# Performance work log

Measured on AMD Instinct MI355X. Metric: run time of the kernel, lower is better.

## Reference

```python
import jax, jax.numpy as jnp
import numpy as np

HEADS = 8
KD = 64  # key_dim
VD = 64  # value_dim


def _conv1x1(W, b, x):
    # 1x1 conv == per-pixel matmul over channels. W: [out, in], x: [b, in, h, w]
    return jnp.einsum('oc,bchw->bohw', W, x) + b[:, None, None]


def setup_inputs() -> dict:
    key = jax.random.key(0)
    ks = jax.random.split(key, 9)
    B, C, H, W = 4, 128, 128, 128
    s = 0.02
    return {
        'x':  jax.random.normal(ks[0], (B, C, H, W), jnp.float32),
        'Wq': jax.random.normal(ks[1], (KD * HEADS, C), jnp.float32) * s,
        'bq': jax.random.normal(ks[2], (KD * HEADS,), jnp.float32) * s,
        'Wk': jax.random.normal(ks[3], (KD * HEADS, C), jnp.float32) * s,
        'bk': jax.random.normal(ks[4], (KD * HEADS,), jnp.float32) * s,
        'Wv': jax.random.normal(ks[5], (VD * HEADS, C), jnp.float32) * s,
        'bv': jax.random.normal(ks[6], (VD * HEADS,), jnp.float32) * s,
        'Wo': jax.random.normal(ks[7], (C, VD * HEADS), jnp.float32) * s,
        'bo': jax.random.normal(ks[8], (C,), jnp.float32) * s,
    }


def reference(x, Wq, bq, Wk, bk, Wv, bv, Wo, bo):
    B, C, H, W = x.shape
    n = H * W
    scale = KD ** -0.25
    # projections -> [b, heads, dim, n]
    q = _conv1x1(Wq, bq, x).reshape(B, HEADS, KD, n) * scale
    k = _conv1x1(Wk, bk, x).reshape(B, HEADS, KD, n) * scale
    v = _conv1x1(Wv, bv, x).reshape(B, HEADS, VD, n)
    # linear attention: softmax k over tokens (n), softmax q over key dim (d)
    k = jax.nn.softmax(k, axis=-1)
    q = jax.nn.softmax(q, axis=-2)
    ctx = jnp.einsum('bhdn,bhen->bhde', k, v)   # [b, h, kd, vd] small context
    out = jnp.einsum('bhdn,bhde->bhen', q, ctx)  # [b, h, vd, n]
    out = out.reshape(B, HEADS * VD, H, W)
    return _conv1x1(Wo, bo, out)
```

## Files before the change

### kernel.cpp

```cpp
#include <hip/hip_runtime.h>

typedef unsigned short u16;
typedef __bf16 bf16x8 __attribute__((ext_vector_type(8)));
typedef float f32x4 __attribute__((ext_vector_type(4)));

#define N_ 16384
#define SCALE 0.35355339059327379f

__device__ __forceinline__ u16 f2bf(float f){
  union { float f; unsigned int i; } v; v.f = f;
  unsigned int b = v.i;
  return (u16)((b + 0x7FFFu + ((b >> 16) & 1u)) >> 16);
}
__device__ __forceinline__ unsigned int cvtpk(float a, float b){
  unsigned int r;
  asm("v_cvt_pk_bf16_f32 %0, %1, %2" : "=v"(r) : "v"(a), "v"(b));
  return r;
}

__global__ __launch_bounds__(256) void pconvx(const float* __restrict__ x,
    u16* __restrict__ xt, const float* __restrict__ Wq,
    const float* __restrict__ bq, const float* __restrict__ Wk,
    const float* __restrict__ bk, const float* __restrict__ Wv,
    const float* __restrict__ bv, u16* __restrict__ wkvf, u16* __restrict__ wqf,
    float* __restrict__ bkv, float* __restrict__ bqs){
  const int tid = threadIdx.x;
  const int bid = blockIdx.x;
  if (bid < 512){
    const int b = bid >> 7;
    const int kq = tid >> 6;
    const int t0 = (bid & 127) * 128 + 2 * (tid & 63);
    const float* xp = x + (size_t)(b * 128 + kq * 32) * N_ + t0;
    u16* dst = xt + (size_t)(b * N_ + t0) * 128;
#pragma unroll
    for (int gi = 0; gi < 4; gi++){
      float2 v[8];
#pragma unroll
      for (int j = 0; j < 8; j++)
        v[j] = *(const float2*)(xp + (size_t)(gi * 8 + j) * N_);
      const int g = kq * 4 + gi;
      {
        uint4 o;
        o.x = cvtpk(v[0].x, v[1].x); o.y = cvtpk(v[2].x, v[3].x);
        o.z = cvtpk(v[4].x, v[5].x); o.w = cvtpk(v[6].x, v[7].x);
        *(uint4*)(dst + ((g ^ (t0 & 15)) * 8)) = o;
      }
      {
        uint4 o;
        o.x = cvtpk(v[0].y, v[1].y); o.y = cvtpk(v[2].y, v[3].y);
        o.z = cvtpk(v[4].y, v[5].y); o.w = cvtpk(v[6].y, v[7].y);
        const int t = t0 + 1;
        *(uint4*)(dst + 128 + ((g ^ (t & 15)) * 8)) = o;
      }
    }
    return;
  }
  const int T = (bid - 512) * 256 + tid;
  if (T < 1024){
    int jj = T & 127, h = T >> 7;
    bkv[T] = (jj < 64) ? SCALE * bk[h * 64 + jj] : bv[h * 64 + jj - 64];
  } else if (T < 1536){
    bqs[T - 1024] = SCALE * bq[T - 1024];
  }
  const float* src; float sc; u16* dst;
  if (T < 16384){
    int l = T & 63, f = T >> 6;
    int ks = f & 3, jt = (f >> 2) & 7, h = f >> 5;
    int jj = 16 * jt + (l & 15);
    int k0 = ks * 32 + (l >> 4) * 8;
    if (jj < 64){ src = Wk + (size_t)(h * 64 + jj) * 128 + k0; sc = SCALE; }
    else        { src = Wv + (size_t)(h * 64 + jj - 64) * 128 + k0; sc = 1.f; }
    dst = wkvf + (size_t)f * 512 + l * 8;
  } else {
    int T2 = T - 16384;
    int l = T2 & 63, f = T2 >> 6;
    int ks = f & 3, dt = (f >> 2) & 3, h = f >> 4;
    int d = 16 * dt + (l & 15);
    int k0 = ks * 32 + (l >> 4) * 8;
    src = Wq + (size_t)(h * 64 + d) * 128 + k0; sc = SCALE;
    dst = wqf + (size_t)f * 512 + l * 8;
  }
  float4 a = *(const float4*)src, c = *(const float4*)(src + 4);
  ushort4 o0, o1;
  o0.x = f2bf(sc * a.x); o0.y = f2bf(sc * a.y); o0.z = f2bf(sc * a.z); o0.w = f2bf(sc * a.w);
  o1.x = f2bf(sc * c.x); o1.y = f2bf(sc * c.y); o1.z = f2bf(sc * c.z); o1.w = f2bf(sc * c.w);
  *(ushort4*)dst = o0; *(ushort4*)(dst + 4) = o1;
}

__global__ __launch_bounds__(256, 2) void kvctx(const u16* __restrict__ xt,
    const u16* __restrict__ wkvf, const float* __restrict__ bkv,
    float* __restrict__ pctx, float* __restrict__ prs){
  __shared__ u16 smem[32768];
  const int tid = threadIdx.x;
  const int chunk = blockIdx.x, h = blockIdx.y, b = blockIdx.z;
  const int w = tid >> 6, l = tid & 63, r15 = l & 15, q = l >> 4;
  const int th = w & 1, jh = w >> 1;

  bf16x8 wf[4][4];
#pragma unroll
  for (int ni = 0; ni < 4; ni++)
#pragma unroll
    for (int ks = 0; ks < 4; ks++)
      wf[ni][ks] = *(const bf16x8*)(wkvf +
          (size_t)((h * 8 + 4 * jh + ni) * 4 + ks) * 512 + l * 8);
  float barr[4];
#pragma unroll
  for (int ni = 0; ni < 4; ni++)
    barr[ni] = bkv[h * 128 + jh * 64 + 16 * ni + r15];

  const size_t tok0 = (size_t)b * N_ + chunk * 512;
  const char* gbase = (const char*)(xt + tok0 * 128);
  u16* sekv = smem + 16384;

#define STAGE(sub_)                                                            \
  {                                                                            \
    const char* gs = gbase + (size_t)(sub_)*32768 + w * 8192 + l * 16;         \
    char* ls = (char*)smem + w * 8192;                                         \
    _Pragma("unroll")                                                          \
    for (int p = 0; p < 8; p++)                                                \
      __builtin_amdgcn_global_load_lds(                                        \
          (const __attribute__((address_space(1))) void*)(gs + p * 1024),      \
          (__attribute__((address_space(3))) void*)(ls + p * 1024), 16, 0, 0); \
  }

  STAGE(0);
  __syncthreads();

  f32x4 acc2[4][4] = {};
  float rs[4] = {0.f, 0.f, 0.f, 0.f};

  for (int sub = 0; sub < 4; sub++){
    f32x4 acc1[4][4] = {};
#pragma unroll
    for (int ks = 0; ks < 4; ks++){
      bf16x8 xa[4];
#pragma unroll
      for (int mi = 0; mi < 4; mi++){
        int t = th * 64 + 16 * mi + r15;
        xa[mi] = *(const bf16x8*)&smem[t * 128 + (((ks * 4 + q) ^ r15) * 8)];
      }
#pragma unroll
      for (int mi = 0; mi < 4; mi++)
#pragma unroll
        for (int ni = 0; ni < 4; ni++)
          acc1[mi][ni] = __builtin_amdgcn_mfma_f32_16x16x32_bf16(
              xa[mi], wf[ni][ks], acc1[mi][ni], 0, 0, 0);
    }
    asm volatile("s_waitcnt lgkmcnt(0)" ::: "memory");
    __builtin_amdgcn_s_barrier();
    if (sub < 3) STAGE(sub + 1);
#pragma unroll
    for (int ni = 0; ni < 4; ni++){
      const float bb = barr[ni];
      const int j = jh * 64 + 16 * ni + r15;
      float ps = 0.f;
#pragma unroll
      for (int mi = 0; mi < 4; mi++){
        float vals[4];
#pragma unroll
        for (int r = 0; r < 4; r++) vals[r] = acc1[mi][ni][r] + bb;
        if (jh == 0){
#pragma unroll
          for (int r = 0; r < 4; r++){ vals[r] = __expf(vals[r]); ps += vals[r]; }
        }
        uint2 pk;
        pk.x = cvtpk(vals[0], vals[1]);
        pk.y = cvtpk(vals[2], vals[3]);
        int g8 = 16 * th + 4 * mi + q;
        int g8s = g8 ^ (2 * r15);
        *(uint2*)&sekv[j * 128 + g8s * 4] = pk;
      }
      if (jh == 0){
        ps += __shfl_xor(ps, 16); ps += __shfl_xor(ps, 32);
        rs[ni] += ps;
      }
    }
    asm volatile("s_waitcnt lgkmcnt(0)" ::: "memory");
    __builtin_amdgcn_s_barrier();
    {
      bf16x8 ka[4], va[4];
      const int g8s = (8 * w + 2 * q) ^ (2 * r15);
#pragma unroll
      for (int mi2 = 0; mi2 < 4; mi2++){
        int d = 16 * mi2 + r15;
        ka[mi2] = *(const bf16x8*)&sekv[d * 128 + g8s * 4];
      }
#pragma unroll
      for (int ni2 = 0; ni2 < 4; ni2++){
        int e = 16 * ni2 + r15;
        va[ni2] = *(const bf16x8*)&sekv[(64 + e) * 128 + g8s * 4];
      }
#pragma unroll
      for (int mi2 = 0; mi2 < 4; mi2++)
#pragma unroll
        for (int ni2 = 0; ni2 < 4; ni2++)
          acc2[mi2][ni2] = __builtin_amdgcn_mfma_f32_16x16x32_bf16(
              ka[mi2], va[ni2], acc2[mi2][ni2], 0, 0, 0);
    }
    __syncthreads();
  }
#undef STAGE
  float* fb = (float*)smem;
#pragma unroll
  for (int mi2 = 0; mi2 < 4; mi2++)
#pragma unroll
    for (int ni2 = 0; ni2 < 4; ni2++)
#pragma unroll
      for (int r = 0; r < 4; r++){
        int d = 16 * mi2 + 4 * q + r, e = 16 * ni2 + r15;
        fb[w * 4096 + d * 64 + e] = acc2[mi2][ni2][r];
      }
  __syncthreads();
  {
    float* dst = pctx + ((size_t)((b * 8 + h) * 32 + chunk)) * 4096 + tid * 16;
#pragma unroll
    for (int i = 0; i < 4; i++){
      int o = tid * 16 + 4 * i;
      float4 a = *(const float4*)(fb + o);
      float4 c = *(const float4*)(fb + 4096 + o);
      float4 d = *(const float4*)(fb + 8192 + o);
      float4 e = *(const float4*)(fb + 12288 + o);
      float4 s;
      s.x = a.x + c.x + d.x + e.x; s.y = a.y + c.y + d.y + e.y;
      s.z = a.z + c.z + d.z + e.z; s.w = a.w + c.w + d.w + e.w;
      *(float4*)(dst + 4 * i) = s;
    }
  }
  if (jh == 0 && q == 0){
    float* rb = prs + ((size_t)((b * 8 + h) * 32 + chunk)) * 128 + th * 64;
#pragma unroll
    for (int ni = 0; ni < 4; ni++) rb[16 * ni + r15] = rs[ni];
  }
}

__global__ __launch_bounds__(256) void redmker(const float* __restrict__ pctx,
    const float* __restrict__ prs, const float* __restrict__ Wo,
    u16* __restrict__ mtf){
  __shared__ float ctxh8[8][68];
  __shared__ float woht[64][132];
  __shared__ float rsh[8];
  const int tid = threadIdx.x;
  const int bh = blockIdx.x, s = blockIdx.y;
  const int h = bh & 7;
  {
    const int e4 = tid & 15, r0 = tid >> 4;
#pragma unroll
    for (int p = 0; p < 8; p++){
      int c = r0 + p * 16;
      float4 v = *(const float4*)(Wo + (size_t)c * 512 + h * 64 + 4 * e4);
      woht[4 * e4 + 0][c] = v.x; woht[4 * e4 + 1][c] = v.y;
      woht[4 * e4 + 2][c] = v.z; woht[4 * e4 + 3][c] = v.w;
    }
  }
  {
    const float* base = pctx + (size_t)bh * 131072 + s * 512 + tid * 2;
    float2 a = {0.f, 0.f};
#pragma unroll 4
    for (int c = 0; c < 32; c++){
      float2 v = *(const float2*)(base + c * 4096);
      a.x += v.x; a.y += v.y;
    }
    const int i = tid * 2;
    ctxh8[i >> 6][i & 63] = a.x;
    ctxh8[(i + 1) >> 6][(i + 1) & 63] = a.y;
  }
  {
    const int dl = tid >> 5, c = tid & 31;
    const int dg = s * 8 + dl;
    const float* rb = prs + (size_t)bh * 4096 + c * 128;
    float v = rb[dg] + rb[64 + dg];
    v += __shfl_xor(v, 1);  v += __shfl_xor(v, 2);
    v += __shfl_xor(v, 4);  v += __shfl_xor(v, 8);
    v += __shfl_xor(v, 16);
    if (c == 0) rsh[dl] = v;
  }
  __syncthreads();
  const int dl = tid >> 5, c0 = (tid & 31) * 4;
  const int d = s * 8 + dl;
  const float inv = 1.f / rsh[dl];
  float acc[4] = {0.f, 0.f, 0.f, 0.f};
  for (int e = 0; e < 64; e++){
    float cv = ctxh8[dl][e];
#pragma unroll
    for (int j = 0; j < 4; j++) acc[j] += cv * woht[e][c0 + j];
  }
  const int ks = d >> 5, lq = ((d >> 3) & 3) << 4, el = d & 7;
#pragma unroll
  for (int j = 0; j < 4; j++){
    int c = c0 + j;
    mtf[((size_t)(bh * 8 + (c >> 4)) * 2 + ks) * 512 + ((c & 15) | lq) * 8 + el]
        = f2bf(inv * acc[j]);
  }
}

__global__ __launch_bounds__(256, 3) void qout(const u16* __restrict__ xt,
    const u16* __restrict__ wqf, const float* __restrict__ bqs,
    const u16* __restrict__ mtf, const float* __restrict__ bo,
    float* __restrict__ out){
  __shared__ u16 smWq[8192];
  __shared__ u16 smWm[8192];
  __shared__ u16 smP[4][16 * 64];
  const int tid = threadIdx.x;
  const int tt = blockIdx.x, b = blockIdx.y;
  const int w = tid >> 6, l = tid & 63, r15 = l & 15, q = l >> 4;
  const int t0 = tt * 64;
  const int m7 = 2 * (r15 & 7);
  const int t = t0 + w * 16 + r15;

  bf16x8 xb[4];
#pragma unroll
  for (int ks = 0; ks < 4; ks++)
    xb[ks] = *(const bf16x8*)(xt + (size_t)(b * N_ + t) * 128 +
                              (((ks * 4 + q) ^ r15) * 8));

  u16* sp = smP[w];
  f32x4 acc3[8] = {};
  for (int h = 0; h < 8; h++){
    {
      const char* gsrc = (w < 2)
          ? (const char*)(wqf + (size_t)h * 8192) + w * 8192 + l * 16
          : (const char*)(mtf + (size_t)(b * 8 + h) * 8192) + (w - 2) * 8192 + l * 16;
      char* ldst = (w < 2) ? (char*)smWq + w * 8192
                           : (char*)smWm + (w - 2) * 8192;
#pragma unroll
      for (int p = 0; p < 8; p++)
        __builtin_amdgcn_global_load_lds(
            (const __attribute__((address_space(1))) void*)(gsrc + p * 1024),
            (__attribute__((address_space(3))) void*)(ldst + p * 1024), 16, 0, 0);
    }
    __syncthreads();

    float bq_[4][4];
#pragma unroll
    for (int mi = 0; mi < 4; mi++){
      float4 v = *(const float4*)(bqs + h * 64 + 16 * mi + 4 * q);
      bq_[mi][0] = v.x; bq_[mi][1] = v.y; bq_[mi][2] = v.z; bq_[mi][3] = v.w;
    }
    f32x4 acc1[4] = {};
#pragma unroll
    for (int ks = 0; ks < 4; ks++){
      bf16x8 wqv[4];
#pragma unroll
      for (int mi = 0; mi < 4; mi++)
        wqv[mi] = *(const bf16x8*)&smWq[(mi * 4 + ks) * 512 + l * 8];
#pragma unroll
      for (int mi = 0; mi < 4; mi++)
        acc1[mi] = __builtin_amdgcn_mfma_f32_16x16x32_bf16(
            wqv[mi], xb[ks], acc1[mi], 0, 0, 0);
    }
    {
      float ps = 0.f;
#pragma unroll
      for (int mi = 0; mi < 4; mi++)
#pragma unroll
        for (int r = 0; r < 4; r++){
          float e = __expf(acc1[mi][r] + bq_[mi][r]);
          acc1[mi][r] = e; ps += e;
        }
      ps += __shfl_xor(ps, 16); ps += __shfl_xor(ps, 32);
      const float ci = 1.f / ps;
#pragma unroll
      for (int mi = 0; mi < 4; mi++){
        uint2 pk;
        pk.x = cvtpk(acc1[mi][0] * ci, acc1[mi][1] * ci);
        pk.y = cvtpk(acc1[mi][2] * ci, acc1[mi][3] * ci);
        int g8s = (4 * mi + q) ^ m7;
        *(uint2*)&sp[r15 * 64 + g8s * 4] = pk;
      }
    }
#pragma unroll
    for (int ks2 = 0; ks2 < 2; ks2++){
      const int g8s = (8 * ks2 + 2 * q) ^ m7;
      bf16x8 pb = *(const bf16x8*)&sp[r15 * 64 + g8s * 4];
#pragma unroll
      for (int mm = 0; mm < 8; mm++){
        bf16x8 mf = *(const bf16x8*)&smWm[(mm * 2 + ks2) * 512 + l * 8];
        acc3[mm] = __builtin_amdgcn_mfma_f32_16x16x32_bf16(
            mf, pb, acc3[mm], 0, 0, 0);
      }
    }
    if (h < 7) __syncthreads();
  }
#pragma unroll
  for (int mi = 0; mi < 8; mi++){
    float4 bv = *(const float4*)(bo + 16 * mi + 4 * q);
    float bs[4] = {bv.x, bv.y, bv.z, bv.w};
#pragma unroll
    for (int r = 0; r < 4; r++){
      int c = 16 * mi + 4 * q + r;
      out[(size_t)(b * 128 + c) * N_ + t] = acc3[mi][r] + bs[r];
    }
  }
}

extern "C" void kernel_launch(void* const* d_in, const int* in_sizes, int n_in,
                              void* d_out, int out_size, void* d_ws, size_t ws_size,
                              hipStream_t stream){
  const float* x  = (const float*)d_in[0];
  const float* Wq = (const float*)d_in[1];
  const float* bq = (const float*)d_in[2];
  const float* Wk = (const float*)d_in[3];
  const float* bk = (const float*)d_in[4];
  const float* Wv = (const float*)d_in[5];
  const float* bv = (const float*)d_in[6];
  const float* Wo = (const float*)d_in[7];
  const float* bo = (const float*)d_in[8];
  float* out = (float*)d_out;

  char* ws = (char*)d_ws;
  u16*   xt     = (u16*)ws;
  u16*   wkvf   = (u16*)(ws + 16777216);
  u16*   wqf    = (u16*)(ws + 17039360);
  u16*   mtf    = (u16*)(ws + 17170432);
  float* bkv    = (float*)(ws + 17694720);
  float* bqs    = (float*)(ws + 17698816);
  float* pctx   = (float*)(ws + 18233344);
  float* prs    = (float*)(ws + 35010560);

  pconvx <<<608, 256, 0, stream>>>(x, xt, Wq, bq, Wk, bk, Wv, bv,
                                   wkvf, wqf, bkv, bqs);
  kvctx  <<<dim3(32, 8, 4), 256, 0, stream>>>(xt, wkvf, bkv, pctx, prs);
  redmker<<<dim3(32, 8), 256, 0, stream>>>(pctx, prs, Wo, mtf);
  qout   <<<dim3(256, 4), 256, 0, stream>>>(xt, wqf, bqs, mtf, bo, out);
}
```

Measured before the change: 170.5 us.

## Halve kvctx grid with larger token chunks and balance softmax exp across waves

Each kvctx block now processes 1024 tokens (8 sub-stages) instead of 512, so the grid shrinks from 32 to 16 chunks per (b,h). This halves the partial-context writes and the reduction reads in redmker. Output-column tiles are also reassigned so every wave handles two K tiles (which need exp) and two V tiles. Previously only half the waves did all the exp work. The cost is fewer blocks (512 total), which may under-fill the GPU, and a longer serial loop per block.

New measurement: 163.6 us, median of 2. 1.04x faster.

```diff
diff --git a/kernel.cpp b/kernel.cpp
--- a/kernel.cpp
+++ b/kernel.cpp
@@ -92,23 +92,27 @@
     float* __restrict__ pctx, float* __restrict__ prs){
   __shared__ u16 smem[32768];
   const int tid = threadIdx.x;
-  const int chunk = blockIdx.x, h = blockIdx.y, b = blockIdx.z;
+  const int cp = blockIdx.x, h = blockIdx.y, b = blockIdx.z;
   const int w = tid >> 6, l = tid & 63, r15 = l & 15, q = l >> 4;
   const int th = w & 1, jh = w >> 1;
 
+  int jt_[4];
+#pragma unroll
+  for (int ni = 0; ni < 4; ni++) jt_[ni] = (ni < 2) ? (2 * jh + ni) : (2 + 2 * jh + ni);
+
   bf16x8 wf[4][4];
 #pragma unroll
   for (int ni = 0; ni < 4; ni++)
 #pragma unroll
     for (int ks = 0; ks < 4; ks++)
       wf[ni][ks] = *(const bf16x8*)(wkvf +
-          (size_t)((h * 8 + 4 * jh + ni) * 4 + ks) * 512 + l * 8);
+          (size_t)((h * 8 + jt_[ni]) * 4 + ks) * 512 + l * 8);
   float barr[4];
 #pragma unroll
   for (int ni = 0; ni < 4; ni++)
-    barr[ni] = bkv[h * 128 + jh * 64 + 16 * ni + r15];
-
-  const size_t tok0 = (size_t)b * N_ + chunk * 512;
+    barr[ni] = bkv[h * 128 + jt_[ni] * 16 + r15];
+
+  const size_t tok0 = (size_t)b * N_ + cp * 1024;
   const char* gbase = (const char*)(xt + tok0 * 128);
   u16* sekv = smem + 16384;
 
@@ -127,9 +131,9 @@
   __syncthreads();
 
   f32x4 acc2[4][4] = {};
-  float rs[4] = {0.f, 0.f, 0.f, 0.f};
-
-  for (int sub = 0; sub < 4; sub++){
+  float rs[2] = {0.f, 0.f};
+
+  for (int sub = 0; sub < 8; sub++){
     f32x4 acc1[4][4] = {};
 #pragma unroll
     for (int ks = 0; ks < 4; ks++){
@@ -148,18 +152,18 @@
     }
     asm volatile("s_waitcnt lgkmcnt(0)" ::: "memory");
     __builtin_amdgcn_s_barrier();
-    if (sub < 3) STAGE(sub + 1);
+    if (sub < 7) STAGE(sub + 1);
 #pragma unroll
     for (int ni = 0; ni < 4; ni++){
       const float bb = barr[ni];
-      const int j = jh * 64 + 16 * ni + r15;
+      const int j = jt_[ni] * 16 + r15;
       float ps = 0.f;
 #pragma unroll
       for (int mi = 0; mi < 4; mi++){
         float vals[4];
 #pragma unroll
         for (int r = 0; r < 4; r++) vals[r] = acc1[mi][ni][r] + bb;
-        if (jh == 0){
+        if (ni < 2){
 #pragma unroll
           for (int r = 0; r < 4; r++){ vals[r] = __expf(vals[r]); ps += vals[r]; }
         }
@@ -170,7 +174,7 @@
         int g8s = g8 ^ (2 * r15);
         *(uint2*)&sekv[j * 128 + g8s * 4] = pk;
       }
-      if (jh == 0){
+      if (ni < 2){
         ps += __shfl_xor(ps, 16); ps += __shfl_xor(ps, 32);
         rs[ni] += ps;
       }
@@ -212,7 +216,7 @@
       }
   __syncthreads();
   {
-    float* dst = pctx + ((size_t)((b * 8 + h) * 32 + chunk)) * 4096 + tid * 16;
+    float* dst = pctx + ((size_t)((b * 8 + h) * 16 + cp)) * 4096 + tid * 16;
 #pragma unroll
     for (int i = 0; i < 4; i++){
       int o = tid * 16 + 4 * i;
@@ -226,10 +230,10 @@
       *(float4*)(dst + 4 * i) = s;
     }
   }
-  if (jh == 0 && q == 0){
-    float* rb = prs + ((size_t)((b * 8 + h) * 32 + chunk)) * 128 + th * 64;
-#pragma unroll
-    for (int ni = 0; ni < 4; ni++) rb[16 * ni + r15] = rs[ni];
+  if (q == 0){
+    float* rb = prs + ((size_t)((b * 8 + h) * 16 + cp)) * 128 + th * 64 + 32 * jh;
+#pragma unroll
+    for (int ni = 0; ni < 2; ni++) rb[16 * ni + r15] = rs[ni];
   }
 }
 
@@ -253,10 +257,10 @@
     }
   }
   {
-    const float* base = pctx + (size_t)bh * 131072 + s * 512 + tid * 2;
+    const float* base = pctx + (size_t)bh * 65536 + s * 512 + tid * 2;
     float2 a = {0.f, 0.f};
 #pragma unroll 4
-    for (int c = 0; c < 32; c++){
+    for (int c = 0; c < 16; c++){
       float2 v = *(const float2*)(base + c * 4096);
       a.x += v.x; a.y += v.y;
     }
@@ -267,8 +271,11 @@
   {
     const int dl = tid >> 5, c = tid & 31;
     const int dg = s * 8 + dl;
-    const float* rb = prs + (size_t)bh * 4096 + c * 128;
-    float v = rb[dg] + rb[64 + dg];
+    float v = 0.f;
+    if (c < 16){
+      const float* rb = prs + (size_t)bh * 2048 + c * 128;
+      v = rb[dg] + rb[64 + dg];
+    }
     v += __shfl_xor(v, 1);  v += __shfl_xor(v, 2);
     v += __shfl_xor(v, 4);  v += __shfl_xor(v, 8);
     v += __shfl_xor(v, 16);
@@ -419,7 +426,7 @@
 
   pconvx <<<608, 256, 0, stream>>>(x, xt, Wq, bq, Wk, bk, Wv, bv,
                                    wkvf, wqf, bkv, bqs);
-  kvctx  <<<dim3(32, 8, 4), 256, 0, stream>>>(xt, wkvf, bkv, pctx, prs);
+  kvctx  <<<dim3(16, 8, 4), 256, 0, stream>>>(xt, wkvf, bkv, pctx, prs);
   redmker<<<dim3(32, 8), 256, 0, stream>>>(pctx, prs, Wo, mtf);
   qout   <<<dim3(256, 4), 256, 0, stream>>>(xt, wqf, bqs, mtf, bo, out);
 }
```
